# Optimization experiments

Measured on AMD Instinct MI355X. Metric: run time of the kernel, lower is better.

Reference implementation:

```python
import jax, jax.numpy as jnp
import numpy as np
from jax import lax

B, C, H, W = 16, 128, 64, 64
S = 16  # d_state


def setup_inputs() -> dict:
    key = jax.random.key(0)
    ks = jax.random.split(key, 12)
    d = {
        'x': jax.random.normal(ks[0], (B, C, H, W), jnp.float32),
        'conv_w': jax.random.normal(ks[1], (C, C, 3, 3), jnp.float32) * (1.0 / np.sqrt(C * 9)),
        'conv_b': jax.random.normal(ks[2], (C,), jnp.float32) * 0.01,
        'dt_w': jax.random.normal(ks[3], (C, C), jnp.float32) * (1.0 / np.sqrt(C)),
        'dt_b': jax.random.normal(ks[4], (C,), jnp.float32) * 0.01,
        'A': jax.random.normal(ks[5], (C, S), jnp.float32),
        'D': jax.random.normal(ks[6], (C,), jnp.float32),
        'g1_w': jax.random.normal(ks[7], (C, C), jnp.float32) * (1.0 / np.sqrt(C)),
        'g1_b': jax.random.normal(ks[8], (C,), jnp.float32) * 0.01,
        'g2_w': jax.random.normal(ks[9], (C, C), jnp.float32) * (1.0 / np.sqrt(C)),
        'g2_b': jax.random.normal(ks[10], (C,), jnp.float32) * 0.01,
    }
    return d


def _forward(x, conv_w, conv_b, dt_w, dt_b, A, D, g1_w, g1_b, g2_w, g2_b):
    identity = x
    # 3x3 conv, padding=1 (SAME)
    x = lax.conv_general_dilated(x, conv_w, (1, 1), 'SAME',
                                 dimension_numbers=('NCHW', 'OIHW', 'NCHW'))
    x = x + conv_b[None, :, None, None]
    # spectral gate: global avg pool -> 1x1 conv -> relu -> 1x1 conv -> sigmoid
    pooled = jnp.mean(x, axis=(2, 3))                       # [B, C]
    g = jax.nn.relu(jnp.einsum('bc,oc->bo', pooled, g1_w) + g1_b)
    g = jax.nn.sigmoid(jnp.einsum('bc,oc->bo', g, g2_w) + g2_b)
    x = x * g[:, :, None, None]
    # ssm scan over H*W tokens
    x_seq = x.transpose(0, 2, 3, 1).reshape(x.shape[0], H * W, C)  # [B, L, C]
    dt = jax.nn.sigmoid(jnp.einsum('blc,oc->blo', x_seq, dt_w) + dt_b)
    An = -jnp.exp(A)   # [C, S]
    Dp = jnp.exp(D)    # [C]

    def step(h, inp):
        xt, dtt = inp  # each [B, C]
        h = h * jnp.exp(An[None] * dtt[:, :, None]) + xt[:, :, None]  # [B, C, S]
        y = jnp.sum(h * An[None], axis=-1) + Dp * xt                   # [B, C]
        return h, y

    h0 = jnp.zeros((x.shape[0], C, S), x.dtype)
    xs = (x_seq.transpose(1, 0, 2), dt.transpose(1, 0, 2))  # [L, B, C]
    _, ys = lax.scan(step, h0, xs)                           # ys: [L, B, C]
    y = ys.transpose(1, 0, 2).reshape(x.shape[0], H, W, C).transpose(0, 3, 1, 2)
    return y + identity


def reference(x, conv_w, conv_b, dt_w, dt_b, A, D, g1_w, g1_b, g2_w, g2_b):
    return _forward(x, conv_w, conv_b, dt_w, dt_b, A, D, g1_w, g1_b, g2_w, g2_b)
```

## Files before the change

### kernel.cpp

```cpp
#include <hip/hip_runtime.h>
#include <hip/hip_bf16.h>
#include <stdint.h>

#define BB 16
#define CC 128
#define HH 64
#define WW 64
#define LL 4096
#define SS 16
#define NCH 64
#define CT 64

typedef __attribute__((ext_vector_type(4))) float f32x4;
typedef __attribute__((ext_vector_type(8))) short short8;
typedef __attribute__((ext_vector_type(4))) unsigned int u32x4;

#define AS1 __attribute__((address_space(1)))
#define AS3 __attribute__((address_space(3)))

__device__ __forceinline__ float bf2f(unsigned short u) {
    union { unsigned int i; float f; } v;
    v.i = ((unsigned int)u) << 16;
    return v.f;
}
__device__ __forceinline__ unsigned short f2bf(float f) {
    union { float f; unsigned int i; } v;
    v.f = f;
    unsigned int x = v.i;
    return (unsigned short)((x + 0x7fffu + ((x >> 16) & 1u)) >> 16);
}
__device__ __forceinline__ float fexp2(float x) { return __builtin_amdgcn_exp2f(x); }

__global__ void k0a(const float* __restrict__ conv_w, const float* __restrict__ dt_w,
                    const float* __restrict__ A, const float* __restrict__ Dv,
                    short* __restrict__ wf, short* __restrict__ wdtf,
                    float* __restrict__ An, float* __restrict__ An2, float* __restrict__ Dp,
                    float* __restrict__ pooled) {
    int idx = blockIdx.x * 256 + threadIdx.x;
    if (idx < 18432) {
        int lane = idx & 63, fr = idx >> 6;
        int nfg = fr & 7, ks = (fr >> 3) & 3, tp = fr >> 5;
        int dy = tp / 3, dx = tp % 3;
        int cout = nfg * 16 + (lane & 15);
        int cin0 = ks * 32 + (lane >> 4) * 8;
        short8 v;
#pragma unroll
        for (int j = 0; j < 8; ++j)
            v[j] = (short)f2bf(conv_w[((cout * CC + cin0 + j) * 3 + dy) * 3 + dx]);
        *(short8*)(wf + (size_t)idx * 8) = v;
    } else if (idx < 20480) {
        int i2 = idx - 18432;
        int lane = i2 & 63, fr = i2 >> 6;
        int nfg = fr & 7, ks = fr >> 3;
        int o = nfg * 16 + (lane & 15);
        int c0 = ks * 32 + (lane >> 4) * 8;
        short8 v;
#pragma unroll
        for (int j = 0; j < 8; ++j) v[j] = (short)f2bf(dt_w[o * CC + c0 + j]);
        *(short8*)(wdtf + (size_t)i2 * 8) = v;
    } else if (idx < 22528) {
        int i3 = idx - 20480;
        float a = -expf(A[i3]);
        An[i3] = a;
        An2[i3] = a * 1.4426950408889634f;
    } else if (idx < 22656) {
        int c = idx - 22528;
        Dp[c] = expf(Dv[c]);
    } else if (idx < 24704) {
        pooled[idx - 22656] = 0.f;
    }
}

__global__ __launch_bounds__(256) void k0b(const float* __restrict__ x, unsigned short* __restrict__ xT) {
    __shared__ float lt[64][65];
    int bid = blockIdx.x;
    int b = bid >> 7, rem = bid & 127;
    int tt = rem >> 1, ct = rem & 1;
    int t0 = tt * 64, c0 = ct * 64;
    int tid = threadIdx.x;
    int colr = tid & 63, rowb = tid >> 6;
#pragma unroll
    for (int r = 0; r < 16; ++r) {
        int row = rowb + r * 4;
        lt[row][colr] = x[(size_t)(b * CC + c0 + row) * LL + t0 + colr];
    }
    __syncthreads();
#pragma unroll
    for (int r = 0; r < 16; ++r) {
        int trow = rowb + r * 4;
        xT[((size_t)b * LL + t0 + trow) * CC + c0 + colr] = f2bf(lt[colr][trow]);
    }
}

__global__ __launch_bounds__(256) void k1(const unsigned short* __restrict__ xT,
                                          const short* __restrict__ wf,
                                          const float* __restrict__ conv_b,
                                          unsigned short* __restrict__ convT,
                                          float* __restrict__ pooled) {
    __shared__ __align__(16) unsigned short slab[3 * 66 * 128];
    int bid = blockIdx.x;
    int b = bid >> 6, h = bid & 63;
    int tid = threadIdx.x;
    int wave = tid >> 6, lane = tid & 63;

    if (tid < 96) {
        int dy = tid >> 5, r = (tid >> 4) & 1, j = tid & 15;
        u32x4 z = {0, 0, 0, 0};
        *(u32x4*)((char*)slab + dy * 16896 + (r ? 16640 : 0) + j * 16) = z;
    }
#pragma unroll
    for (int dy = 0; dy < 3; ++dy) {
        int hs = h + dy - 1;
        char* slabdy = (char*)slab + dy * 16896;
        if (hs >= 0 && hs < HH) {
            const char* src = (const char*)xT + (size_t)(b * LL + hs * 64) * 256;
#pragma unroll
            for (int i = 0; i < 4; ++i) {
                unsigned int Xbase = 256u + (unsigned)i * 4096u + (unsigned)wave * 1024u;
                unsigned int X = Xbase + (unsigned)lane * 16u;
                unsigned int tok = X >> 8;
                unsigned int srcoff = ((X & ~255u) - 256u) | ((X & 255u) ^ ((tok & 7u) << 4));
                __builtin_amdgcn_global_load_lds((const AS1 unsigned int*)(src + srcoff),
                                                 (AS3 unsigned int*)(slabdy + Xbase), 16, 0, 0);
            }
        } else {
            u32x4 z = {0, 0, 0, 0};
#pragma unroll
            for (int i = 0; i < 4; ++i)
                *(u32x4*)(slabdy + 256 + tid * 64 + i * 16) = z;
        }
    }
    __syncthreads();

    int lm = lane & 15, lg = lane >> 4;
    f32x4 acc[4][2];
#pragma unroll
    for (int m = 0; m < 4; ++m)
#pragma unroll
        for (int n = 0; n < 2; ++n) acc[m][n] = (f32x4){0.f, 0.f, 0.f, 0.f};

#pragma unroll
    for (int tp = 0; tp < 9; ++tp) {
        int dy = tp / 3, dx = tp % 3;
        const char* slabdy = (const char*)slab + dy * 16896;
#pragma unroll
        for (int ks = 0; ks < 4; ++ks) {
            short8 bf0 = *(const short8*)(wf + ((size_t)(((tp * 4 + ks) * 8) + wave * 2 + 0) * 64 + lane) * 8);
            short8 bf1 = *(const short8*)(wf + ((size_t)(((tp * 4 + ks) * 8) + wave * 2 + 1) * 64 + lane) * 8);
#pragma unroll
            for (int mf = 0; mf < 4; ++mf) {
                int tok = mf * 16 + lm + dx;
                unsigned int off = (unsigned)((tok * 256 + ks * 64 + lg * 16) ^ ((tok & 7) << 4));
                short8 af = *(const short8*)(slabdy + off);
                acc[mf][0] = __builtin_amdgcn_mfma_f32_16x16x32_bf16(af, bf0, acc[mf][0], 0, 0, 0);
                acc[mf][1] = __builtin_amdgcn_mfma_f32_16x16x32_bf16(af, bf1, acc[mf][1], 0, 0, 0);
            }
        }
    }

    int n0w = wave * 32;
    size_t tokbase = (size_t)(b * LL + h * 64);
    float psum[2] = {0.f, 0.f};
#pragma unroll
    for (int nf = 0; nf < 2; ++nf) {
        int n = n0w + nf * 16 + lm;
        float bias = conv_b[n];
#pragma unroll
        for (int mf = 0; mf < 4; ++mf)
#pragma unroll
            for (int r = 0; r < 4; ++r) {
                int w = mf * 16 + lg * 4 + r;
                float v = acc[mf][nf][r] + bias;
                convT[(tokbase + w) * CC + n] = f2bf(v);
                psum[nf] += v;
            }
    }
#pragma unroll
    for (int nf = 0; nf < 2; ++nf) {
        float s = psum[nf];
        s += __shfl_xor(s, 16);
        s += __shfl_xor(s, 32);
        if (lane < 16) atomicAdd(&pooled[b * CC + n0w + nf * 16 + lane], s);
    }
}

__global__ __launch_bounds__(128) void k2(const float* __restrict__ pooled, const float* __restrict__ g1w,
                                          const float* __restrict__ g1b, const float* __restrict__ g2w,
                                          const float* __restrict__ g2b, float* __restrict__ gate) {
    __shared__ float wl[128 * 129];
    __shared__ float meanr[128];
    __shared__ float garr[128];
    int b = blockIdx.x;
    int tid = threadIdx.x;
    meanr[tid] = pooled[b * CC + tid] * (1.f / 4096.f);
#pragma unroll 4
    for (int i = 0; i < 128; ++i) wl[i * 129 + tid] = g1w[i * 128 + tid];
    __syncthreads();
    float acc = g1b[tid];
    for (int c = 0; c < 128; ++c) acc += meanr[c] * wl[tid * 129 + c];
    garr[tid] = fmaxf(acc, 0.f);
    __syncthreads();
#pragma unroll 4
    for (int i = 0; i < 128; ++i) wl[i * 129 + tid] = g2w[i * 128 + tid];
    __syncthreads();
    float acc2 = g2b[tid];
    for (int c = 0; c < 128; ++c) acc2 += garr[c] * wl[tid * 129 + c];
    gate[b * CC + tid] = __builtin_amdgcn_rcpf(1.f + fexp2(-1.4426950408889634f * acc2));
}

__global__ __launch_bounds__(256) void k3(const unsigned short* __restrict__ convT,
                                          const short* __restrict__ wdtf,
                                          const float* __restrict__ gate,
                                          const float* __restrict__ dt_b,
                                          const float* __restrict__ An2,
                                          unsigned short* __restrict__ dtT,
                                          float* __restrict__ hend, float* __restrict__ decay) {
    __shared__ __align__(16) unsigned short albuf[128 * 128];
    __shared__ __align__(16) unsigned short dtl[128 * 136];
    __shared__ float gl[128];
    int bid = blockIdx.x;
    int b = bid >> 5, tile = bid & 31, t0 = tile * 128;
    int tid = threadIdx.x;
    int wave = tid >> 6, lane = tid & 63;
    if (tid < 128) gl[tid] = gate[b * CC + tid];
    __syncthreads();
    const char* srcb = (const char*)convT + (size_t)(b * LL + t0) * 256;
#pragma unroll
    for (int i = 0; i < 8; ++i) {
        unsigned int byteoff = (unsigned)((i * 256 + tid) * 16);
        unsigned int tok = byteoff >> 8;
        unsigned int inner = byteoff & 255u;
        int c8 = (int)(inner >> 1);
        short8 v = *(const short8*)(srcb + (size_t)tok * 256 + inner);
#pragma unroll
        for (int j = 0; j < 8; ++j) {
            float f = bf2f((unsigned short)v[j]) * gl[c8 + j];
            v[j] = (short)f2bf(f);
        }
        *(short8*)((char*)albuf + (byteoff ^ ((tok & 7u) << 4))) = v;
    }
    __syncthreads();

    int lm = lane & 15, lg = lane >> 4;
    f32x4 acc[8][2];
#pragma unroll
    for (int m = 0; m < 8; ++m)
#pragma unroll
        for (int n = 0; n < 2; ++n) acc[m][n] = (f32x4){0.f, 0.f, 0.f, 0.f};
#pragma unroll
    for (int ks = 0; ks < 4; ++ks) {
        short8 bf0 = *(const short8*)(wdtf + ((size_t)((ks * 8) + wave * 2 + 0) * 64 + lane) * 8);
        short8 bf1 = *(const short8*)(wdtf + ((size_t)((ks * 8) + wave * 2 + 1) * 64 + lane) * 8);
#pragma unroll
        for (int mf = 0; mf < 8; ++mf) {
            int tok = mf * 16 + lm;
            unsigned int off = (unsigned)((tok * 256 + ks * 64 + lg * 16) ^ ((tok & 7) << 4));
            short8 af = *(const short8*)((const char*)albuf + off);
            acc[mf][0] = __builtin_amdgcn_mfma_f32_16x16x32_bf16(af, bf0, acc[mf][0], 0, 0, 0);
            acc[mf][1] = __builtin_amdgcn_mfma_f32_16x16x32_bf16(af, bf1, acc[mf][1], 0, 0, 0);
        }
    }
#pragma unroll
    for (int nf = 0; nf < 2; ++nf) {
        int o = wave * 32 + nf * 16 + lm;
        float zb = dt_b[o];
#pragma unroll
        for (int mf = 0; mf < 8; ++mf)
#pragma unroll
            for (int r = 0; r < 4; ++r) {
                int tok = mf * 16 + lg * 4 + r;
                float z = acc[mf][nf][r] + zb;
                float d = __builtin_amdgcn_rcpf(1.f + fexp2(-1.4426950408889634f * z));
                unsigned short ub = f2bf(d);
                dtT[(size_t)(b * LL + t0 + tok) * CC + o] = ub;
                dtl[tok * 136 + o] = ub;
            }
    }
    __syncthreads();

    int half = tid >> 7, c = tid & 127;
    int ch = tile * 2 + half;
    float a2[SS], h[SS];
#pragma unroll
    for (int s = 0; s < SS; ++s) {
        a2[s] = An2[c * SS + s];
        h[s] = 0.f;
    }
    float sdt = 0.f;
#pragma unroll 4
    for (int t = 0; t < CT; ++t) {
        int tokb = half * 64 + t;
        unsigned int xoff = ((unsigned)(tokb * 256 + c * 2)) ^ (((unsigned)tokb & 7u) << 4);
        float x = bf2f(*(const unsigned short*)((const char*)albuf + xoff));
        float d = bf2f(dtl[tokb * 136 + c]);
        sdt += d;
#pragma unroll
        for (int s = 0; s < SS; ++s) h[s] = h[s] * fexp2(a2[s] * d) + x;
    }
    size_t base = ((size_t)(b * NCH + ch) * CC + c) * SS;
#pragma unroll
    for (int q = 0; q < 4; ++q) {
        f32x4 hv, dv;
#pragma unroll
        for (int j = 0; j < 4; ++j) {
            hv[j] = h[q * 4 + j];
            dv[j] = fexp2(a2[q * 4 + j] * sdt);
        }
        *(f32x4*)(hend + base + q * 4) = hv;
        *(f32x4*)(decay + base + q * 4) = dv;
    }
}

__global__ __launch_bounds__(256) void k5(const float* __restrict__ hend, const float* __restrict__ decay,
                                          float* __restrict__ H0) {
    int idx = blockIdx.x * 256 + threadIdx.x;
    int b = idx >> 11, rem = idx & 2047;
    float Hv = 0.f;
    for (int k = 0; k < NCH; ++k) {
        size_t base = (size_t)(b * NCH + k) * 2048 + rem;
        H0[base] = Hv;
        Hv = hend[base] + Hv * decay[base];
    }
}

__global__ __launch_bounds__(128) void k6(const unsigned short* __restrict__ convT,
                                          const unsigned short* __restrict__ dtT,
                                          const float* __restrict__ gate,
                                          const float* __restrict__ Antab,
                                          const float* __restrict__ An2tab,
                                          const float* __restrict__ Dp,
                                          const float* __restrict__ H0,
                                          const float* __restrict__ xin,
                                          float* __restrict__ out) {
    __shared__ float ylds[128][65];
    int bid = blockIdx.x;
    int b = bid >> 6, ch = bid & 63;
    int c = threadIdx.x;
    float a2[SS], an[SS], h[SS];
#pragma unroll
    for (int s = 0; s < SS; ++s) {
        a2[s] = An2tab[c * SS + s];
        an[s] = Antab[c * SS + s];
    }
    size_t hbase = ((size_t)(b * NCH + ch) * CC + c) * SS;
#pragma unroll
    for (int s = 0; s < SS; ++s) h[s] = H0[hbase + s];
    float g = gate[b * CC + c];
    float dpc = Dp[c];
    int t0 = ch * CT;
    const unsigned short* xp = convT + (size_t)(b * LL + t0) * CC + c;
    const unsigned short* dp = dtT + (size_t)(b * LL + t0) * CC + c;
#pragma unroll 4
    for (int t = 0; t < CT; ++t) {
        float x = bf2f(xp[t * CC]) * g;
        float d = bf2f(dp[t * CC]);
        float y = dpc * x;
#pragma unroll
        for (int s = 0; s < SS; ++s) {
            h[s] = h[s] * fexp2(a2[s] * d) + x;
            y += h[s] * an[s];
        }
        ylds[c][t] = y;
    }
    __syncthreads();
    int tt = c & 63, rh = c >> 6;
    size_t outbase = (size_t)b * CC * LL + t0 + tt;
#pragma unroll 4
    for (int rr = 0; rr < 64; ++rr) {
        int row = rr * 2 + rh;
        size_t gi = outbase + (size_t)row * LL;
        out[gi] = ylds[row][tt] + xin[gi];
    }
}

extern "C" void kernel_launch(void* const* d_in, const int* in_sizes, int n_in,
                              void* d_out, int out_size, void* d_ws, size_t ws_size,
                              hipStream_t stream) {
    const float* x      = (const float*)d_in[0];
    const float* conv_w = (const float*)d_in[1];
    const float* conv_b = (const float*)d_in[2];
    const float* dt_w   = (const float*)d_in[3];
    const float* dt_b   = (const float*)d_in[4];
    const float* A      = (const float*)d_in[5];
    const float* D      = (const float*)d_in[6];
    const float* g1w    = (const float*)d_in[7];
    const float* g1b    = (const float*)d_in[8];
    const float* g2w    = (const float*)d_in[9];
    const float* g2b    = (const float*)d_in[10];

    char* ws = (char*)d_ws;
    unsigned short* xT    = (unsigned short*)(ws + 0);
    float* hend           = (float*)(ws + 0);
    float* decay          = (float*)(ws + 8388608);
    unsigned short* convT = (unsigned short*)(ws + 16777216);
    unsigned short* dtT   = (unsigned short*)(ws + 33554432);
    float* H0             = (float*)(ws + 50331648);
    short* wf             = (short*)(ws + 58720256);
    short* wdtf           = (short*)(ws + 59015168);
    float* pooled         = (float*)(ws + 59047936);
    float* gate           = (float*)(ws + 59056128);
    float* Antab          = (float*)(ws + 59064320);
    float* An2tab         = (float*)(ws + 59072512);
    float* Dp             = (float*)(ws + 59080704);
    float* outp           = (float*)d_out;

    hipLaunchKernelGGL(k0a, dim3(97), dim3(256), 0, stream, conv_w, dt_w, A, D, wf, wdtf, Antab, An2tab, Dp, pooled);
    hipLaunchKernelGGL(k0b, dim3(2048), dim3(256), 0, stream, x, xT);
    hipLaunchKernelGGL(k1, dim3(1024), dim3(256), 0, stream, xT, wf, conv_b, convT, pooled);
    hipLaunchKernelGGL(k2, dim3(16), dim3(128), 0, stream, pooled, g1w, g1b, g2w, g2b, gate);
    hipLaunchKernelGGL(k3, dim3(512), dim3(256), 0, stream, convT, wdtf, gate, dt_b, An2tab, dtT, hend, decay);
    hipLaunchKernelGGL(k5, dim3(128), dim3(256), 0, stream, hend, decay, H0);
    hipLaunchKernelGGL(k6, dim3(1024), dim3(128), 0, stream, convT, dtT, gate, Antab, An2tab, Dp, H0, x, outp);
}
```

Baseline: 135.1 us.

## Merge prep kernels, fuse gate MLP into dt GEMM, stage scan inputs via LDS

Merges the weight-prep and input-transpose kernels into one launch, which also pre-transposes the gate MLP weights. The separate gate kernel is removed and every dt-projection block recomputes the spectral gate from the pooled sums, removing two launches at the cost of redundant per-block MLP work. The scan kernel now stages its convT and dtT chunk into LDS with global_load_lds, loads H0 as vectors, and keeps the scan output in bf16 in LDS, trading some precision on y for less LDS and faster strided reads. H0 and the transposed gate weights share workspace memory, which relies on k5 writing H0 only after k3 has finished reading those weights.

```diff
diff --git a/kernel.cpp b/kernel.cpp
--- a/kernel.cpp
+++ b/kernel.cpp
@@ -31,12 +31,35 @@
 }
 __device__ __forceinline__ float fexp2(float x) { return __builtin_amdgcn_exp2f(x); }
 
-__global__ void k0a(const float* __restrict__ conv_w, const float* __restrict__ dt_w,
-                    const float* __restrict__ A, const float* __restrict__ Dv,
-                    short* __restrict__ wf, short* __restrict__ wdtf,
-                    float* __restrict__ An, float* __restrict__ An2, float* __restrict__ Dp,
-                    float* __restrict__ pooled) {
-    int idx = blockIdx.x * 256 + threadIdx.x;
+__global__ __launch_bounds__(256) void k0(const float* __restrict__ x, unsigned short* __restrict__ xT,
+                                          const float* __restrict__ conv_w, const float* __restrict__ dt_w,
+                                          const float* __restrict__ A, const float* __restrict__ Dv,
+                                          const float* __restrict__ g1w, const float* __restrict__ g2w,
+                                          short* __restrict__ wf, short* __restrict__ wdtf,
+                                          float* __restrict__ An, float* __restrict__ An2, float* __restrict__ Dp,
+                                          float* __restrict__ pooled, float* __restrict__ g1wT, float* __restrict__ g2wT) {
+    __shared__ float lt[64][65];
+    int bid = blockIdx.x;
+    int tid = threadIdx.x;
+    if (bid < 2048) {
+        int b = bid >> 7, rem = bid & 127;
+        int tt = rem >> 1, ct = rem & 1;
+        int t0 = tt * 64, c0 = ct * 64;
+        int colr = tid & 63, rowb = tid >> 6;
+#pragma unroll
+        for (int r = 0; r < 16; ++r) {
+            int row = rowb + r * 4;
+            lt[row][colr] = x[(size_t)(b * CC + c0 + row) * LL + t0 + colr];
+        }
+        __syncthreads();
+#pragma unroll
+        for (int r = 0; r < 16; ++r) {
+            int trow = rowb + r * 4;
+            xT[((size_t)b * LL + t0 + trow) * CC + c0 + colr] = f2bf(lt[colr][trow]);
+        }
+        return;
+    }
+    int idx = (bid - 2048) * 256 + tid;
     if (idx < 18432) {
         int lane = idx & 63, fr = idx >> 6;
         int nfg = fr & 7, ks = (fr >> 3) & 3, tp = fr >> 5;
@@ -68,27 +91,14 @@
         Dp[c] = expf(Dv[c]);
     } else if (idx < 24704) {
         pooled[idx - 22656] = 0.f;
-    }
-}
-
-__global__ __launch_bounds__(256) void k0b(const float* __restrict__ x, unsigned short* __restrict__ xT) {
-    __shared__ float lt[64][65];
-    int bid = blockIdx.x;
-    int b = bid >> 7, rem = bid & 127;
-    int tt = rem >> 1, ct = rem & 1;
-    int t0 = tt * 64, c0 = ct * 64;
-    int tid = threadIdx.x;
-    int colr = tid & 63, rowb = tid >> 6;
-#pragma unroll
-    for (int r = 0; r < 16; ++r) {
-        int row = rowb + r * 4;
-        lt[row][colr] = x[(size_t)(b * CC + c0 + row) * LL + t0 + colr];
-    }
-    __syncthreads();
-#pragma unroll
-    for (int r = 0; r < 16; ++r) {
-        int trow = rowb + r * 4;
-        xT[((size_t)b * LL + t0 + trow) * CC + c0 + colr] = f2bf(lt[colr][trow]);
+    } else if (idx < 41088) {
+        int i = idx - 24704;
+        int c = i >> 7, o = i & 127;
+        g1wT[i] = g1w[o * 128 + c];
+    } else if (idx < 57472) {
+        int i = idx - 41088;
+        int c = i >> 7, o = i & 127;
+        g2wT[i] = g2w[o * 128 + c];
     }
 }
 
@@ -184,33 +194,12 @@
     }
 }
 
-__global__ __launch_bounds__(128) void k2(const float* __restrict__ pooled, const float* __restrict__ g1w,
-                                          const float* __restrict__ g1b, const float* __restrict__ g2w,
-                                          const float* __restrict__ g2b, float* __restrict__ gate) {
-    __shared__ float wl[128 * 129];
-    __shared__ float meanr[128];
-    __shared__ float garr[128];
-    int b = blockIdx.x;
-    int tid = threadIdx.x;
-    meanr[tid] = pooled[b * CC + tid] * (1.f / 4096.f);
-#pragma unroll 4
-    for (int i = 0; i < 128; ++i) wl[i * 129 + tid] = g1w[i * 128 + tid];
-    __syncthreads();
-    float acc = g1b[tid];
-    for (int c = 0; c < 128; ++c) acc += meanr[c] * wl[tid * 129 + c];
-    garr[tid] = fmaxf(acc, 0.f);
-    __syncthreads();
-#pragma unroll 4
-    for (int i = 0; i < 128; ++i) wl[i * 129 + tid] = g2w[i * 128 + tid];
-    __syncthreads();
-    float acc2 = g2b[tid];
-    for (int c = 0; c < 128; ++c) acc2 += garr[c] * wl[tid * 129 + c];
-    gate[b * CC + tid] = __builtin_amdgcn_rcpf(1.f + fexp2(-1.4426950408889634f * acc2));
-}
-
 __global__ __launch_bounds__(256) void k3(const unsigned short* __restrict__ convT,
                                           const short* __restrict__ wdtf,
-                                          const float* __restrict__ gate,
+                                          const float* __restrict__ pooled,
+                                          const float* __restrict__ g1wT, const float* __restrict__ g1b,
+                                          const float* __restrict__ g2wT, const float* __restrict__ g2b,
+                                          float* __restrict__ gate,
                                           const float* __restrict__ dt_b,
                                           const float* __restrict__ An2,
                                           unsigned short* __restrict__ dtT,
@@ -218,12 +207,30 @@
     __shared__ __align__(16) unsigned short albuf[128 * 128];
     __shared__ __align__(16) unsigned short dtl[128 * 136];
     __shared__ float gl[128];
+    float* meanr = (float*)dtl;
+    float* garr  = ((float*)dtl) + 128;
     int bid = blockIdx.x;
     int b = bid >> 5, tile = bid & 31, t0 = tile * 128;
     int tid = threadIdx.x;
     int wave = tid >> 6, lane = tid & 63;
-    if (tid < 128) gl[tid] = gate[b * CC + tid];
-    __syncthreads();
+
+    if (tid < 128) meanr[tid] = pooled[b * CC + tid] * (1.f / 4096.f);
+    __syncthreads();
+    if (tid < 128) {
+        float acc = g1b[tid];
+        for (int c = 0; c < 128; ++c) acc += meanr[c] * g1wT[c * 128 + tid];
+        garr[tid] = fmaxf(acc, 0.f);
+    }
+    __syncthreads();
+    if (tid < 128) {
+        float acc2 = g2b[tid];
+        for (int c = 0; c < 128; ++c) acc2 += garr[c] * g2wT[c * 128 + tid];
+        float gv = __builtin_amdgcn_rcpf(1.f + fexp2(-1.4426950408889634f * acc2));
+        gl[tid] = gv;
+        if (tile == 0) gate[b * CC + tid] = gv;
+    }
+    __syncthreads();
+
     const char* srcb = (const char*)convT + (size_t)(b * LL + t0) * 256;
 #pragma unroll
     for (int i = 0; i < 8; ++i) {
@@ -260,6 +267,7 @@
             acc[mf][1] = __builtin_amdgcn_mfma_f32_16x16x32_bf16(af, bf1, acc[mf][1], 0, 0, 0);
         }
     }
+    __syncthreads();
 #pragma unroll
     for (int nf = 0; nf < 2; ++nf) {
         int o = wave * 32 + nf * 16 + lm;
@@ -332,10 +340,27 @@
                                           const float* __restrict__ H0,
                                           const float* __restrict__ xin,
                                           float* __restrict__ out) {
-    __shared__ float ylds[128][65];
+    __shared__ __align__(16) unsigned short xl[64 * 128];
+    __shared__ __align__(16) unsigned short dl[64 * 128];
+    __shared__ unsigned short ylds[128][66];
     int bid = blockIdx.x;
     int b = bid >> 6, ch = bid & 63;
-    int c = threadIdx.x;
+    int tid = threadIdx.x;
+    int wave = tid >> 6, lane = tid & 63;
+    int t0 = ch * CT;
+
+    const char* xsrc = (const char*)convT + (size_t)(b * LL + t0) * 256;
+    const char* dsrc = (const char*)dtT + (size_t)(b * LL + t0) * 256;
+#pragma unroll
+    for (int i = 0; i < 8; ++i) {
+        unsigned int off = (unsigned)(i * 2048 + wave * 1024);
+        __builtin_amdgcn_global_load_lds((const AS1 unsigned int*)(xsrc + off + lane * 16u),
+                                         (AS3 unsigned int*)((char*)xl + off), 16, 0, 0);
+        __builtin_amdgcn_global_load_lds((const AS1 unsigned int*)(dsrc + off + lane * 16u),
+                                         (AS3 unsigned int*)((char*)dl + off), 16, 0, 0);
+    }
+
+    int c = tid;
     float a2[SS], an[SS], h[SS];
 #pragma unroll
     for (int s = 0; s < SS; ++s) {
@@ -344,32 +369,36 @@
     }
     size_t hbase = ((size_t)(b * NCH + ch) * CC + c) * SS;
 #pragma unroll
-    for (int s = 0; s < SS; ++s) h[s] = H0[hbase + s];
+    for (int q = 0; q < 4; ++q) {
+        f32x4 hv = *(const f32x4*)(H0 + hbase + q * 4);
+#pragma unroll
+        for (int j = 0; j < 4; ++j) h[q * 4 + j] = hv[j];
+    }
     float g = gate[b * CC + c];
     float dpc = Dp[c];
-    int t0 = ch * CT;
-    const unsigned short* xp = convT + (size_t)(b * LL + t0) * CC + c;
-    const unsigned short* dp = dtT + (size_t)(b * LL + t0) * CC + c;
+    __syncthreads();
+
 #pragma unroll 4
     for (int t = 0; t < CT; ++t) {
-        float x = bf2f(xp[t * CC]) * g;
-        float d = bf2f(dp[t * CC]);
+        float x = bf2f(xl[t * 128 + c]) * g;
+        float d = bf2f(dl[t * 128 + c]);
         float y = dpc * x;
 #pragma unroll
         for (int s = 0; s < SS; ++s) {
             h[s] = h[s] * fexp2(a2[s] * d) + x;
             y += h[s] * an[s];
         }
-        ylds[c][t] = y;
-    }
-    __syncthreads();
-    int tt = c & 63, rh = c >> 6;
+        ylds[c][t] = f2bf(y);
+    }
+    __syncthreads();
+
+    int tt = lane;
     size_t outbase = (size_t)b * CC * LL + t0 + tt;
 #pragma unroll 4
     for (int rr = 0; rr < 64; ++rr) {
-        int row = rr * 2 + rh;
+        int row = rr * 2 + wave;
         size_t gi = outbase + (size_t)row * LL;
-        out[gi] = ylds[row][tt] + xin[gi];
+        out[gi] = bf2f(ylds[row][tt]) + xin[gi];
     }
 }
 
@@ -395,6 +424,8 @@
     unsigned short* convT = (unsigned short*)(ws + 16777216);
     unsigned short* dtT   = (unsigned short*)(ws + 33554432);
     float* H0             = (float*)(ws + 50331648);
+    float* g1wT           = (float*)(ws + 50331648);
+    float* g2wT           = (float*)(ws + 50397184);
     short* wf             = (short*)(ws + 58720256);
     short* wdtf           = (short*)(ws + 59015168);
     float* pooled         = (float*)(ws + 59047936);
@@ -404,11 +435,11 @@
     float* Dp             = (float*)(ws + 59080704);
     float* outp           = (float*)d_out;
 
-    hipLaunchKernelGGL(k0a, dim3(97), dim3(256), 0, stream, conv_w, dt_w, A, D, wf, wdtf, Antab, An2tab, Dp, pooled);
-    hipLaunchKernelGGL(k0b, dim3(2048), dim3(256), 0, stream, x, xT);
+    hipLaunchKernelGGL(k0, dim3(2273), dim3(256), 0, stream, x, xT, conv_w, dt_w, A, D, g1w, g2w,
+                       wf, wdtf, Antab, An2tab, Dp, pooled, g1wT, g2wT);
     hipLaunchKernelGGL(k1, dim3(1024), dim3(256), 0, stream, xT, wf, conv_b, convT, pooled);
-    hipLaunchKernelGGL(k2, dim3(16), dim3(128), 0, stream, pooled, g1w, g1b, g2w, g2b, gate);
-    hipLaunchKernelGGL(k3, dim3(512), dim3(256), 0, stream, convT, wdtf, gate, dt_b, An2tab, dtT, hend, decay);
+    hipLaunchKernelGGL(k3, dim3(512), dim3(256), 0, stream, convT, wdtf, pooled, g1wT, g1b, g2wT, g2b,
+                       gate, dt_b, An2tab, dtT, hend, decay);
     hipLaunchKernelGGL(k5, dim3(128), dim3(256), 0, stream, hend, decay, H0);
     hipLaunchKernelGGL(k6, dim3(1024), dim3(128), 0, stream, convT, dtT, gate, Antab, An2tab, Dp, H0, x, outp);
 }
```

New measurement: 129.7 us. 4.0% less time.
